# Kernel optimization log

Measured on AMD Instinct MI355X. Metric: run time of the kernel, lower is better.

The kernel has to match this reference:

```python
import jax, jax.numpy as jnp
import numpy as np

N = 100000
E = 1600000
IN_DIM, HID_DIM, LAT_DIM = 256, 128, 64


def glorot(key, shape):
    lim = float(np.sqrt(6.0 / (shape[0] + shape[1])))
    return jax.random.uniform(key, shape, jnp.float32, -lim, lim)


def setup_inputs() -> dict:
    key = jax.random.key(0)
    ks = jax.random.split(key, 8)
    x = jax.random.normal(ks[0], (N, IN_DIM), jnp.float32)
    edge_index = jax.random.randint(ks[1], (2, E), 0, N, jnp.int64)
    return {
        "x": x,
        "edge_index": edge_index,
        "W1": glorot(ks[2], (IN_DIM, HID_DIM)),
        "b1": jnp.zeros((HID_DIM,), jnp.float32),
        "Wmu": glorot(ks[3], (HID_DIM, LAT_DIM)),
        "bmu": jnp.zeros((LAT_DIM,), jnp.float32),
        "Wls": glorot(ks[4], (HID_DIM, LAT_DIM)),
        "bls": jnp.zeros((LAT_DIM,), jnp.float32),
    }


def gcn_conv(x, src, dst, norm, W, b, n_nodes):
    # PyG GCNConv: linear transform, then symmetric-normalized scatter-add
    h = x @ W                                   # [N, out]
    msg = h[src] * norm[:, None]                # [E+N, out] gathered messages
    out = jax.ops.segment_sum(msg, dst, num_segments=n_nodes)
    return out + b


def reference(x, edge_index, W1, b1, Wmu, bmu, Wls, bls):
    # add self-loops (GCNConv default)
    loop = jnp.arange(N, dtype=edge_index.dtype)
    src = jnp.concatenate([edge_index[0], loop])
    dst = jnp.concatenate([edge_index[1], loop])
    # symmetric degree normalization: deg computed on target nodes
    deg = jax.ops.segment_sum(jnp.ones_like(dst, jnp.float32), dst, num_segments=N)
    dinv = jnp.where(deg > 0, jax.lax.rsqrt(jnp.maximum(deg, 1.0)), 0.0)
    norm = dinv[src] * dinv[dst]                # [E+N]

    h = jax.nn.relu(gcn_conv(x, src, dst, norm, W1, b1, N))
    mu = gcn_conv(h, src, dst, norm, Wmu, bmu, N)
    logstd = gcn_conv(h, src, dst, norm, Wls, bls, N)
    return (mu, logstd)
```

## Files before the change

### kernel.cpp

```cpp
#include <hip/hip_runtime.h>

#define IN_DIM 256
#define HID    128
#define LAT    64
#define SLOTS  64
#define NBKT   16

typedef __attribute__((ext_vector_type(8))) short short8;
typedef __attribute__((ext_vector_type(4))) float floatx4;
typedef __attribute__((ext_vector_type(4))) int  intx4;
typedef __attribute__((ext_vector_type(2))) int  intx2;

static __device__ __forceinline__ ushort f2bf(float f) {
    union { float f; uint u; } v; v.f = f;
    uint u = v.u;
    uint r = (u + 0x7fffu + ((u >> 16) & 1u)) >> 16;
    return (ushort)r;
}
static __device__ __forceinline__ float bf_lo(uint v) { return __uint_as_float(v << 16); }
static __device__ __forceinline__ float bf_hi(uint v) { return __uint_as_float(v & 0xffff0000u); }

__global__ __launch_bounds__(256) void scatter_kernel(const int* __restrict__ src,
                                                      const int* __restrict__ dst,
                                                      int* __restrict__ bkt,
                                                      int* __restrict__ bkt_cnt,
                                                      int cap, int N, int E) {
    __shared__ int cntL[NBKT], baseL[NBKT], posL[NBKT];
    const int t = threadIdx.x;
    if (t < NBKT) { cntL[t] = 0; posL[t] = 0; }
    __syncthreads();
    const float sc = (float)NBKT / (float)N;
    const int e0 = blockIdx.x * 2048 + t * 8;
    int s[8], d[8];
    if (e0 + 7 < E) {
        *(int4*)(s)     = *(const int4*)(src + e0);
        *(int4*)(s + 4) = *(const int4*)(src + e0 + 4);
        *(int4*)(d)     = *(const int4*)(dst + e0);
        *(int4*)(d + 4) = *(const int4*)(dst + e0 + 4);
    } else {
        #pragma unroll
        for (int k = 0; k < 8; ++k) {
            int e = e0 + k;
            s[k] = (e < E) ? src[e] : 0;
            d[k] = (e < E) ? dst[e] : -1;
        }
    }
    int r[8];
    #pragma unroll
    for (int k = 0; k < 8; ++k) {
        r[k] = (d[k] >= 0) ? min((int)((float)d[k] * sc), NBKT - 1) : -1;
        if (r[k] >= 0) atomicAdd(&cntL[r[k]], 1);
    }
    __syncthreads();
    if (t < NBKT) baseL[t] = atomicAdd(&bkt_cnt[t], cntL[t]);
    __syncthreads();
    #pragma unroll
    for (int k = 0; k < 8; ++k) {
        if (r[k] >= 0) {
            int off = atomicAdd(&posL[r[k]], 1);
            int p = baseL[r[k]] + off;
            if (p < cap) {
                intx2 pk; pk.x = s[k]; pk.y = d[k];
                __builtin_nontemporal_store(pk,
                    (intx2*)(bkt + ((size_t)r[k] * cap + p) * 2));
            }
        }
    }
}

__global__ __launch_bounds__(256) void fill_kernel(const int* __restrict__ bkt,
                                                   const int* __restrict__ bkt_cnt,
                                                   int* __restrict__ cur,
                                                   int* __restrict__ csr, int cap) {
    const int xcd  = blockIdx.x & 7;
    const int slot = blockIdx.x >> 3;
    const int bpx  = gridDim.x >> 3;
    for (int ph = 0; ph < NBKT / 8; ++ph) {
        const int r  = ph * 8 + xcd;
        const int sz = min(bkt_cnt[r], cap);
        const int* b = bkt + (size_t)r * cap * 2;
        for (int i = (slot * 256 + threadIdx.x) * 4; i + 3 < sz; i += bpx * 1024) {
            intx4 e01 = __builtin_nontemporal_load((const intx4*)(b + (size_t)i * 2));
            intx4 e23 = __builtin_nontemporal_load((const intx4*)(b + (size_t)i * 2 + 4));
            int p0 = atomicAdd(&cur[e01.y], 1);
            int p1 = atomicAdd(&cur[e01.w], 1);
            int p2 = atomicAdd(&cur[e23.y], 1);
            int p3 = atomicAdd(&cur[e23.w], 1);
            if (p0 < SLOTS) csr[(e01.y << 6) + p0] = e01.x;
            if (p1 < SLOTS) csr[(e01.w << 6) + p1] = e01.z;
            if (p2 < SLOTS) csr[(e23.y << 6) + p2] = e23.x;
            if (p3 < SLOTS) csr[(e23.w << 6) + p3] = e23.z;
        }
        if (slot == 0) {
            int k = (sz & ~3) + threadIdx.x;
            if (k < sz) {
                int es = b[(size_t)k * 2];
                int ed = b[(size_t)k * 2 + 1];
                int p = atomicAdd(&cur[ed], 1);
                if (p < SLOTS) csr[(ed << 6) + p] = es;
            }
        }
    }
}

__global__ __launch_bounds__(256) void dinv_kernel(const int* __restrict__ cur,
                                                   float* __restrict__ dinv, int N) {
    int i = blockIdx.x * 256 + threadIdx.x;
    if (i < N) dinv[i] = rsqrtf((float)(cur[i] + 1));
}

__global__ void prep_weights(const float* __restrict__ W1, const float* __restrict__ Wmu,
                             const float* __restrict__ Wls,
                             ushort* __restrict__ W1T, ushort* __restrict__ W2T) {
    int idx = blockIdx.x * 256 + threadIdx.x;
    if (idx < IN_DIM * HID) {
        int n = idx & 127, k = idx >> 7;
        W1T[n * IN_DIM + k] = f2bf(W1[idx]);
    } else {
        int j = idx - IN_DIM * HID;
        if (j < HID * LAT) {
            int n = j & 63, k = j >> 6;
            W2T[n * HID + k] = f2bf(Wmu[j]);
        } else {
            int jj = j - HID * LAT;
            int n = jj & 63, k = jj >> 6;
            W2T[(64 + n) * HID + k] = f2bf(Wls[jj]);
        }
    }
}

__global__ __launch_bounds__(256) void gemm1_mfma(const float* __restrict__ X,
                                                  const ushort* __restrict__ W1T,
                                                  ushort* __restrict__ O, int N) {
    __shared__ ushort As[64 * 32];
    __shared__ ushort Bs[128 * 32];
    __shared__ ushort Cs[64 * 128];
    const int tid  = threadIdx.x;
    const int wave = tid >> 6, lane = tid & 63;
    const int q = lane >> 4, ln = lane & 15;
    const int row0 = blockIdx.x * 64;
    floatx4 acc[8] = {};

    for (int k0 = 0; k0 < IN_DIM; k0 += 32) {
        #pragma unroll
        for (int t = 0; t < 2; ++t) {
            int j = t * 256 + tid;
            int r = j >> 3, kc = (j & 7) * 4;
            float4 v = make_float4(0.f, 0.f, 0.f, 0.f);
            if (row0 + r < N)
                v = *(const float4*)(X + (size_t)(row0 + r) * IN_DIM + k0 + kc);
            *(ushort4*)(As + r * 32 + kc) =
                make_ushort4(f2bf(v.x), f2bf(v.y), f2bf(v.z), f2bf(v.w));
        }
        #pragma unroll
        for (int t = 0; t < 2; ++t) {
            int c = t * 256 + tid;
            int n = c >> 2, kc = (c & 3) * 8;
            *(int4*)(Bs + n * 32 + kc) = *(const int4*)(W1T + (size_t)n * IN_DIM + k0 + kc);
        }
        __syncthreads();
        short8 a = *(const short8*)(As + (wave * 16 + ln) * 32 + q * 8);
        #pragma unroll
        for (int t = 0; t < 8; ++t) {
            short8 b = *(const short8*)(Bs + (t * 16 + ln) * 32 + q * 8);
            acc[t] = __builtin_amdgcn_mfma_f32_16x16x32_bf16(a, b, acc[t], 0, 0, 0);
        }
        __syncthreads();
    }
    #pragma unroll
    for (int t = 0; t < 8; ++t)
        #pragma unroll
        for (int r = 0; r < 4; ++r)
            Cs[(wave * 16 + q * 4 + r) * 128 + t * 16 + ln] = f2bf(acc[t][r]);
    __syncthreads();
    #pragma unroll
    for (int t = 0; t < 4; ++t) {
        int j = t * 256 + tid;
        int r = j >> 4, c8 = (j & 15) * 8;
        if (row0 + r < N)
            *(int4*)(O + (size_t)(row0 + r) * HID + c8) = *(const int4*)(Cs + r * 128 + c8);
    }
}

__global__ __launch_bounds__(256) void agg_kernel(const ushort* __restrict__ in,
                                                  ushort* __restrict__ out,
                                                  const int* __restrict__ cnt,
                                                  const int* __restrict__ csr,
                                                  const float* __restrict__ dinv,
                                                  const float* __restrict__ bias,
                                                  int N, int mode) {
    int wid  = (blockIdx.x * 256 + threadIdx.x) >> 6;
    int lane = threadIdx.x & 63;
    if (wid >= N) return;
    const int cn   = min(cnt[wid], SLOTS);
    const float dd = dinv[wid];
    int e    = (cn > 0) ? csr[(wid << 6) + min(lane, cn - 1)] : wid;
    float nr = dinv[e] * dd;
    const int q    = lane >> 4;
    const int boff = (lane & 15) * 8;
    const ushort* inb = in + boff;
    float a0=0.f,a1=0.f,a2=0.f,a3=0.f,a4=0.f,a5=0.f,a6=0.f,a7=0.f;
    const int nfull = cn >> 2;
    int jj = 0;
    for (; jj + 2 <= nfull; jj += 2) {
        int j0 = (jj << 2) + q, j1 = j0 + 4;
        int   s0 = __shfl(e,  j0);
        int   s1 = __shfl(e,  j1);
        float n0 = __shfl(nr, j0);
        float n1 = __shfl(nr, j1);
        uint4 v0 = *(const uint4*)(inb + (size_t)s0 * HID);
        uint4 v1 = *(const uint4*)(inb + (size_t)s1 * HID);
        a0 += bf_lo(v0.x) * n0; a1 += bf_hi(v0.x) * n0;
        a2 += bf_lo(v0.y) * n0; a3 += bf_hi(v0.y) * n0;
        a4 += bf_lo(v0.z) * n0; a5 += bf_hi(v0.z) * n0;
        a6 += bf_lo(v0.w) * n0; a7 += bf_hi(v0.w) * n0;
        a0 += bf_lo(v1.x) * n1; a1 += bf_hi(v1.x) * n1;
        a2 += bf_lo(v1.y) * n1; a3 += bf_hi(v1.y) * n1;
        a4 += bf_lo(v1.z) * n1; a5 += bf_hi(v1.z) * n1;
        a6 += bf_lo(v1.w) * n1; a7 += bf_hi(v1.w) * n1;
    }
    if (jj < nfull) {
        int j0 = (jj << 2) + q;
        int   s0 = __shfl(e,  j0);
        float n0 = __shfl(nr, j0);
        uint4 v0 = *(const uint4*)(inb + (size_t)s0 * HID);
        a0 += bf_lo(v0.x) * n0; a1 += bf_hi(v0.x) * n0;
        a2 += bf_lo(v0.y) * n0; a3 += bf_hi(v0.y) * n0;
        a4 += bf_lo(v0.z) * n0; a5 += bf_hi(v0.z) * n0;
        a6 += bf_lo(v0.w) * n0; a7 += bf_hi(v0.w) * n0;
    }
    {
        int rem = cn - (nfull << 2);
        int jT  = max(min((nfull << 2) + q, cn - 1), 0);
        int   sT = __shfl(e,  jT);
        float nT = __shfl(nr, jT);
        if (q < rem) {
            uint4 v0 = *(const uint4*)(inb + (size_t)sT * HID);
            a0 += bf_lo(v0.x) * nT; a1 += bf_hi(v0.x) * nT;
            a2 += bf_lo(v0.y) * nT; a3 += bf_hi(v0.y) * nT;
            a4 += bf_lo(v0.z) * nT; a5 += bf_hi(v0.z) * nT;
            a6 += bf_lo(v0.w) * nT; a7 += bf_hi(v0.w) * nT;
        }
    }
    a0 += __shfl_xor(a0, 16); a1 += __shfl_xor(a1, 16);
    a2 += __shfl_xor(a2, 16); a3 += __shfl_xor(a3, 16);
    a4 += __shfl_xor(a4, 16); a5 += __shfl_xor(a5, 16);
    a6 += __shfl_xor(a6, 16); a7 += __shfl_xor(a7, 16);
    a0 += __shfl_xor(a0, 32); a1 += __shfl_xor(a1, 32);
    a2 += __shfl_xor(a2, 32); a3 += __shfl_xor(a3, 32);
    a4 += __shfl_xor(a4, 32); a5 += __shfl_xor(a5, 32);
    a6 += __shfl_xor(a6, 32); a7 += __shfl_xor(a7, 32);
    if (q == 0) {
        {
            uint4 sv = *(const uint4*)(in + (size_t)wid * HID + boff);
            float ss = dd * dd;
            a0 += bf_lo(sv.x) * ss; a1 += bf_hi(sv.x) * ss;
            a2 += bf_lo(sv.y) * ss; a3 += bf_hi(sv.y) * ss;
            a4 += bf_lo(sv.z) * ss; a5 += bf_hi(sv.z) * ss;
            a6 += bf_lo(sv.w) * ss; a7 += bf_hi(sv.w) * ss;
        }
        if (mode) {
            float4 b0 = *(const float4*)(bias + boff);
            float4 b1 = *(const float4*)(bias + boff + 4);
            a0 = fmaxf(a0 + b0.x, 0.f); a1 = fmaxf(a1 + b0.y, 0.f);
            a2 = fmaxf(a2 + b0.z, 0.f); a3 = fmaxf(a3 + b0.w, 0.f);
            a4 = fmaxf(a4 + b1.x, 0.f); a5 = fmaxf(a5 + b1.y, 0.f);
            a6 = fmaxf(a6 + b1.z, 0.f); a7 = fmaxf(a7 + b1.w, 0.f);
        }
        uint4 pk;
        pk.x = (uint)f2bf(a0) | ((uint)f2bf(a1) << 16);
        pk.y = (uint)f2bf(a2) | ((uint)f2bf(a3) << 16);
        pk.z = (uint)f2bf(a4) | ((uint)f2bf(a5) << 16);
        pk.w = (uint)f2bf(a6) | ((uint)f2bf(a7) << 16);
        *(uint4*)(out + (size_t)wid * HID + boff) = pk;
    }
}

__global__ __launch_bounds__(256) void gemm2_mfma(const ushort* __restrict__ G,
                                                  const ushort* __restrict__ W2T,
                                                  const float* __restrict__ bmu,
                                                  const float* __restrict__ bls,
                                                  float* __restrict__ mu,
                                                  float* __restrict__ ls, int N) {
    __shared__ ushort As[64 * 32];
    __shared__ ushort Bs[128 * 32];
    __shared__ float  Cs[64 * 128];
    const int tid  = threadIdx.x;
    const int wave = tid >> 6, lane = tid & 63;
    const int q = lane >> 4, ln = lane & 15;
    const int row0 = blockIdx.x * 64;
    floatx4 acc[8] = {};

    for (int k0 = 0; k0 < HID; k0 += 32) {
        {
            int r = tid >> 2, kc = (tid & 3) * 8;
            int4 v = make_int4(0, 0, 0, 0);
            if (row0 + r < N) v = *(const int4*)(G + (size_t)(row0 + r) * HID + k0 + kc);
            *(int4*)(As + r * 32 + kc) = v;
        }
        #pragma unroll
        for (int t = 0; t < 2; ++t) {
            int c = t * 256 + tid;
            int n = c >> 2, kc = (c & 3) * 8;
            *(int4*)(Bs + n * 32 + kc) = *(const int4*)(W2T + (size_t)n * HID + k0 + kc);
        }
        __syncthreads();
        short8 a = *(const short8*)(As + (wave * 16 + ln) * 32 + q * 8);
        #pragma unroll
        for (int t = 0; t < 8; ++t) {
            short8 b = *(const short8*)(Bs + (t * 16 + ln) * 32 + q * 8);
            acc[t] = __builtin_amdgcn_mfma_f32_16x16x32_bf16(a, b, acc[t], 0, 0, 0);
        }
        __syncthreads();
    }
    #pragma unroll
    for (int t = 0; t < 8; ++t)
        #pragma unroll
        for (int r = 0; r < 4; ++r)
            Cs[(wave * 16 + q * 4 + r) * 128 + t * 16 + ln] = acc[t][r];
    __syncthreads();
    #pragma unroll
    for (int t = 0; t < 8; ++t) {
        int j = t * 256 + tid;
        int r = j >> 5, c4 = (j & 31) * 4;
        if (row0 + r < N) {
            float4 v = *(const float4*)(Cs + r * 128 + c4);
            if (c4 < 64) {
                float4 b = *(const float4*)(bmu + c4);
                *(float4*)(mu + (size_t)(row0 + r) * LAT + c4) =
                    make_float4(v.x + b.x, v.y + b.y, v.z + b.z, v.w + b.w);
            } else {
                float4 b = *(const float4*)(bls + (c4 - 64));
                *(float4*)(ls + (size_t)(row0 + r) * LAT + (c4 - 64)) =
                    make_float4(v.x + b.x, v.y + b.y, v.z + b.z, v.w + b.w);
            }
        }
    }
}

extern "C" void kernel_launch(void* const* d_in, const int* in_sizes, int n_in,
                              void* d_out, int out_size, void* d_ws, size_t ws_size,
                              hipStream_t stream) {
    const float* x    = (const float*)d_in[0];
    const int*   edge = (const int*)d_in[1];
    const float* W1   = (const float*)d_in[2];
    const float* b1   = (const float*)d_in[3];
    const float* Wmu  = (const float*)d_in[4];
    const float* bmu  = (const float*)d_in[5];
    const float* Wls  = (const float*)d_in[6];
    const float* bls  = (const float*)d_in[7];

    const int N = in_sizes[0] / IN_DIM;
    const int E = in_sizes[1] / 2;
    const int cap = E / NBKT + 8192;

    const int* src = edge;
    const int* dst = edge + E;

    ushort* t1b  = (ushort*)d_ws;
    ushort* hb   = t1b + (size_t)N * HID;
    int*    csr  = (int*)(hb + (size_t)N * HID);
    int*    bkt  = (int*)(csr + (size_t)N * SLOTS);
    float*  dinv = (float*)(bkt + (size_t)NBKT * cap * 2);
    int*    cur  = (int*)(dinv + N);
    int* bkt_cnt = cur + N;
    ushort* W1T  = (ushort*)(bkt_cnt + NBKT);
    ushort* W2T  = W1T + IN_DIM * HID;
    ushort* gb   = t1b;

    float* mu = (float*)d_out;
    float* ls = mu + (size_t)N * LAT;

    (void)hipMemsetAsync(cur, 0, (size_t)(N + NBKT) * sizeof(int), stream);

    scatter_kernel<<<(E + 2047) / 2048, 256, 0, stream>>>(src, dst, bkt, bkt_cnt, cap, N, E);
    fill_kernel<<<1024, 256, 0, stream>>>(bkt, bkt_cnt, cur, csr, cap);
    dinv_kernel<<<(N + 255) / 256, 256, 0, stream>>>(cur, dinv, N);

    prep_weights<<<(IN_DIM * HID + 2 * HID * LAT) / 256, 256, 0, stream>>>(W1, Wmu, Wls, W1T, W2T);
    gemm1_mfma<<<(N + 63) / 64, 256, 0, stream>>>(x, W1T, t1b, N);

    {
        int blocks = (int)(((long long)N * 64 + 255) / 256);
        agg_kernel<<<blocks, 256, 0, stream>>>(t1b, hb, cur, csr, dinv, b1, N, 1);
    }
    {
        int blocks = (int)(((long long)N * 64 + 255) / 256);
        agg_kernel<<<blocks, 256, 0, stream>>>(hb, gb, cur, csr, dinv, nullptr, N, 0);
    }

    gemm2_mfma<<<(N + 63) / 64, 256, 0, stream>>>(gb, W2T, bmu, bls, mu, ls, N);
}
```

Before: 432.5 us.

## Fuse CSR fill with gemm1 and split aggregation across feature halves

Merges the CSR fill kernel and the first MFMA GEMM into a single launch so atomic-bound edge filling overlaps with compute-bound GEMM blocks; prep_weights is moved earlier to feed it. The aggregation kernel now splits each node's 128-wide row into two 64-column halves handled by separate blocks, with each wave processing 8 neighbours per step and an extra shuffle reduction. This aims to cut launch gaps and raise memory-level parallelism in the gather, at the cost of duplicated csr/dinv loads and shorter contiguous reads per neighbour.

```diff
diff --git a/kernel.cpp b/kernel.cpp
--- a/kernel.cpp
+++ b/kernel.cpp
@@ -5,6 +5,7 @@
 #define LAT    64
 #define SLOTS  64
 #define NBKT   16
+#define FILL_BLOCKS 1024
 
 typedef __attribute__((ext_vector_type(8))) short short8;
 typedef __attribute__((ext_vector_type(4))) float floatx4;
@@ -68,38 +69,93 @@
     }
 }
 
-__global__ __launch_bounds__(256) void fill_kernel(const int* __restrict__ bkt,
-                                                   const int* __restrict__ bkt_cnt,
-                                                   int* __restrict__ cur,
-                                                   int* __restrict__ csr, int cap) {
-    const int xcd  = blockIdx.x & 7;
-    const int slot = blockIdx.x >> 3;
-    const int bpx  = gridDim.x >> 3;
-    for (int ph = 0; ph < NBKT / 8; ++ph) {
-        const int r  = ph * 8 + xcd;
-        const int sz = min(bkt_cnt[r], cap);
-        const int* b = bkt + (size_t)r * cap * 2;
-        for (int i = (slot * 256 + threadIdx.x) * 4; i + 3 < sz; i += bpx * 1024) {
-            intx4 e01 = __builtin_nontemporal_load((const intx4*)(b + (size_t)i * 2));
-            intx4 e23 = __builtin_nontemporal_load((const intx4*)(b + (size_t)i * 2 + 4));
-            int p0 = atomicAdd(&cur[e01.y], 1);
-            int p1 = atomicAdd(&cur[e01.w], 1);
-            int p2 = atomicAdd(&cur[e23.y], 1);
-            int p3 = atomicAdd(&cur[e23.w], 1);
-            if (p0 < SLOTS) csr[(e01.y << 6) + p0] = e01.x;
-            if (p1 < SLOTS) csr[(e01.w << 6) + p1] = e01.z;
-            if (p2 < SLOTS) csr[(e23.y << 6) + p2] = e23.x;
-            if (p3 < SLOTS) csr[(e23.w << 6) + p3] = e23.z;
-        }
-        if (slot == 0) {
-            int k = (sz & ~3) + threadIdx.x;
-            if (k < sz) {
-                int es = b[(size_t)k * 2];
-                int ed = b[(size_t)k * 2 + 1];
-                int p = atomicAdd(&cur[ed], 1);
-                if (p < SLOTS) csr[(ed << 6) + p] = es;
+__global__ __launch_bounds__(256) void fill_gemm1_kernel(
+        const int* __restrict__ bkt, const int* __restrict__ bkt_cnt,
+        int* __restrict__ cur, int* __restrict__ csr, int cap,
+        const float* __restrict__ X, const ushort* __restrict__ W1T,
+        ushort* __restrict__ O, int N) {
+    __shared__ ushort As[64 * 32];
+    __shared__ ushort Bs[128 * 32];
+    __shared__ ushort Cs[64 * 128];
+
+    if (blockIdx.x < FILL_BLOCKS) {
+        const int xcd  = blockIdx.x & 7;
+        const int slot = blockIdx.x >> 3;
+        const int bpx  = FILL_BLOCKS >> 3;
+        for (int ph = 0; ph < NBKT / 8; ++ph) {
+            const int r  = ph * 8 + xcd;
+            const int sz = min(bkt_cnt[r], cap);
+            const int* b = bkt + (size_t)r * cap * 2;
+            for (int i = (slot * 256 + threadIdx.x) * 4; i + 3 < sz; i += bpx * 1024) {
+                intx4 e01 = __builtin_nontemporal_load((const intx4*)(b + (size_t)i * 2));
+                intx4 e23 = __builtin_nontemporal_load((const intx4*)(b + (size_t)i * 2 + 4));
+                int p0 = atomicAdd(&cur[e01.y], 1);
+                int p1 = atomicAdd(&cur[e01.w], 1);
+                int p2 = atomicAdd(&cur[e23.y], 1);
+                int p3 = atomicAdd(&cur[e23.w], 1);
+                if (p0 < SLOTS) csr[(e01.y << 6) + p0] = e01.x;
+                if (p1 < SLOTS) csr[(e01.w << 6) + p1] = e01.z;
+                if (p2 < SLOTS) csr[(e23.y << 6) + p2] = e23.x;
+                if (p3 < SLOTS) csr[(e23.w << 6) + p3] = e23.z;
             }
-        }
+            if (slot == 0) {
+                int k = (sz & ~3) + threadIdx.x;
+                if (k < sz) {
+                    int es = b[(size_t)k * 2];
+                    int ed = b[(size_t)k * 2 + 1];
+                    int p = atomicAdd(&cur[ed], 1);
+                    if (p < SLOTS) csr[(ed << 6) + p] = es;
+                }
+            }
+        }
+        return;
+    }
+
+    const int bid  = blockIdx.x - FILL_BLOCKS;
+    const int tid  = threadIdx.x;
+    const int wave = tid >> 6, lane = tid & 63;
+    const int q = lane >> 4, ln = lane & 15;
+    const int row0 = bid * 64;
+    floatx4 acc[8] = {};
+
+    for (int k0 = 0; k0 < IN_DIM; k0 += 32) {
+        #pragma unroll
+        for (int t = 0; t < 2; ++t) {
+            int j = t * 256 + tid;
+            int r = j >> 3, kc = (j & 7) * 4;
+            float4 v = make_float4(0.f, 0.f, 0.f, 0.f);
+            if (row0 + r < N)
+                v = *(const float4*)(X + (size_t)(row0 + r) * IN_DIM + k0 + kc);
+            *(ushort4*)(As + r * 32 + kc) =
+                make_ushort4(f2bf(v.x), f2bf(v.y), f2bf(v.z), f2bf(v.w));
+        }
+        #pragma unroll
+        for (int t = 0; t < 2; ++t) {
+            int c = t * 256 + tid;
+            int n = c >> 2, kc = (c & 3) * 8;
+            *(int4*)(Bs + n * 32 + kc) = *(const int4*)(W1T + (size_t)n * IN_DIM + k0 + kc);
+        }
+        __syncthreads();
+        short8 a = *(const short8*)(As + (wave * 16 + ln) * 32 + q * 8);
+        #pragma unroll
+        for (int t = 0; t < 8; ++t) {
+            short8 b = *(const short8*)(Bs + (t * 16 + ln) * 32 + q * 8);
+            acc[t] = __builtin_amdgcn_mfma_f32_16x16x32_bf16(a, b, acc[t], 0, 0, 0);
+        }
+        __syncthreads();
+    }
+    #pragma unroll
+    for (int t = 0; t < 8; ++t)
+        #pragma unroll
+        for (int r = 0; r < 4; ++r)
+            Cs[(wave * 16 + q * 4 + r) * 128 + t * 16 + ln] = f2bf(acc[t][r]);
+    __syncthreads();
+    #pragma unroll
+    for (int t = 0; t < 4; ++t) {
+        int j = t * 256 + tid;
+        int r = j >> 4, c8 = (j & 15) * 8;
+        if (row0 + r < N)
+            *(int4*)(O + (size_t)(row0 + r) * HID + c8) = *(const int4*)(Cs + r * 128 + c8);
     }
 }
 
@@ -129,59 +185,6 @@
     }
 }
 
-__global__ __launch_bounds__(256) void gemm1_mfma(const float* __restrict__ X,
-                                                  const ushort* __restrict__ W1T,
-                                                  ushort* __restrict__ O, int N) {
-    __shared__ ushort As[64 * 32];
-    __shared__ ushort Bs[128 * 32];
-    __shared__ ushort Cs[64 * 128];
-    const int tid  = threadIdx.x;
-    const int wave = tid >> 6, lane = tid & 63;
-    const int q = lane >> 4, ln = lane & 15;
-    const int row0 = blockIdx.x * 64;
-    floatx4 acc[8] = {};
-
-    for (int k0 = 0; k0 < IN_DIM; k0 += 32) {
-        #pragma unroll
-        for (int t = 0; t < 2; ++t) {
-            int j = t * 256 + tid;
-            int r = j >> 3, kc = (j & 7) * 4;
-            float4 v = make_float4(0.f, 0.f, 0.f, 0.f);
-            if (row0 + r < N)
-                v = *(const float4*)(X + (size_t)(row0 + r) * IN_DIM + k0 + kc);
-            *(ushort4*)(As + r * 32 + kc) =
-                make_ushort4(f2bf(v.x), f2bf(v.y), f2bf(v.z), f2bf(v.w));
-        }
-        #pragma unroll
-        for (int t = 0; t < 2; ++t) {
-            int c = t * 256 + tid;
-            int n = c >> 2, kc = (c & 3) * 8;
-            *(int4*)(Bs + n * 32 + kc) = *(const int4*)(W1T + (size_t)n * IN_DIM + k0 + kc);
-        }
-        __syncthreads();
-        short8 a = *(const short8*)(As + (wave * 16 + ln) * 32 + q * 8);
-        #pragma unroll
-        for (int t = 0; t < 8; ++t) {
-            short8 b = *(const short8*)(Bs + (t * 16 + ln) * 32 + q * 8);
-            acc[t] = __builtin_amdgcn_mfma_f32_16x16x32_bf16(a, b, acc[t], 0, 0, 0);
-        }
-        __syncthreads();
-    }
-    #pragma unroll
-    for (int t = 0; t < 8; ++t)
-        #pragma unroll
-        for (int r = 0; r < 4; ++r)
-            Cs[(wave * 16 + q * 4 + r) * 128 + t * 16 + ln] = f2bf(acc[t][r]);
-    __syncthreads();
-    #pragma unroll
-    for (int t = 0; t < 4; ++t) {
-        int j = t * 256 + tid;
-        int r = j >> 4, c8 = (j & 15) * 8;
-        if (row0 + r < N)
-            *(int4*)(O + (size_t)(row0 + r) * HID + c8) = *(const int4*)(Cs + r * 128 + c8);
-    }
-}
-
 __global__ __launch_bounds__(256) void agg_kernel(const ushort* __restrict__ in,
                                                   ushort* __restrict__ out,
                                                   const int* __restrict__ cnt,
@@ -189,21 +192,23 @@
                                                   const float* __restrict__ dinv,
                                                   const float* __restrict__ bias,
                                                   int N, int mode) {
-    int wid  = (blockIdx.x * 256 + threadIdx.x) >> 6;
-    int lane = threadIdx.x & 63;
+    const int h   = (blockIdx.x >> 2) & 1;
+    const int nb  = (blockIdx.x >> 3) * 4 + (blockIdx.x & 3);
+    const int wid = nb * 4 + (threadIdx.x >> 6);
+    const int lane = threadIdx.x & 63;
     if (wid >= N) return;
     const int cn   = min(cnt[wid], SLOTS);
     const float dd = dinv[wid];
     int e    = (cn > 0) ? csr[(wid << 6) + min(lane, cn - 1)] : wid;
     float nr = dinv[e] * dd;
-    const int q    = lane >> 4;
-    const int boff = (lane & 15) * 8;
+    const int q    = lane >> 3;
+    const int boff = h * 64 + (lane & 7) * 8;
     const ushort* inb = in + boff;
     float a0=0.f,a1=0.f,a2=0.f,a3=0.f,a4=0.f,a5=0.f,a6=0.f,a7=0.f;
-    const int nfull = cn >> 2;
+    const int nfull = cn >> 3;
     int jj = 0;
     for (; jj + 2 <= nfull; jj += 2) {
-        int j0 = (jj << 2) + q, j1 = j0 + 4;
+        int j0 = (jj << 3) + q, j1 = j0 + 8;
         int   s0 = __shfl(e,  j0);
         int   s1 = __shfl(e,  j1);
         float n0 = __shfl(nr, j0);
@@ -220,7 +225,7 @@
         a6 += bf_lo(v1.w) * n1; a7 += bf_hi(v1.w) * n1;
     }
     if (jj < nfull) {
-        int j0 = (jj << 2) + q;
+        int j0 = (jj << 3) + q;
         int   s0 = __shfl(e,  j0);
         float n0 = __shfl(nr, j0);
         uint4 v0 = *(const uint4*)(inb + (size_t)s0 * HID);
@@ -230,8 +235,8 @@
         a6 += bf_lo(v0.w) * n0; a7 += bf_hi(v0.w) * n0;
     }
     {
-        int rem = cn - (nfull << 2);
-        int jT  = max(min((nfull << 2) + q, cn - 1), 0);
+        int rem = cn - (nfull << 3);
+        int jT  = max(min((nfull << 3) + q, cn - 1), 0);
         int   sT = __shfl(e,  jT);
         float nT = __shfl(nr, jT);
         if (q < rem) {
@@ -242,6 +247,10 @@
             a6 += bf_lo(v0.w) * nT; a7 += bf_hi(v0.w) * nT;
         }
     }
+    a0 += __shfl_xor(a0,  8); a1 += __shfl_xor(a1,  8);
+    a2 += __shfl_xor(a2,  8); a3 += __shfl_xor(a3,  8);
+    a4 += __shfl_xor(a4,  8); a5 += __shfl_xor(a5,  8);
+    a6 += __shfl_xor(a6,  8); a7 += __shfl_xor(a7,  8);
     a0 += __shfl_xor(a0, 16); a1 += __shfl_xor(a1, 16);
     a2 += __shfl_xor(a2, 16); a3 += __shfl_xor(a3, 16);
     a4 += __shfl_xor(a4, 16); a5 += __shfl_xor(a5, 16);
@@ -374,18 +383,21 @@
     (void)hipMemsetAsync(cur, 0, (size_t)(N + NBKT) * sizeof(int), stream);
 
     scatter_kernel<<<(E + 2047) / 2048, 256, 0, stream>>>(src, dst, bkt, bkt_cnt, cap, N, E);
-    fill_kernel<<<1024, 256, 0, stream>>>(bkt, bkt_cnt, cur, csr, cap);
+    prep_weights<<<(IN_DIM * HID + 2 * HID * LAT) / 256, 256, 0, stream>>>(W1, Wmu, Wls, W1T, W2T);
+
+    {
+        int g1Blocks = (N + 63) / 64;
+        fill_gemm1_kernel<<<FILL_BLOCKS + g1Blocks, 256, 0, stream>>>(
+            bkt, bkt_cnt, cur, csr, cap, x, W1T, t1b, N);
+    }
     dinv_kernel<<<(N + 255) / 256, 256, 0, stream>>>(cur, dinv, N);
 
-    prep_weights<<<(IN_DIM * HID + 2 * HID * LAT) / 256, 256, 0, stream>>>(W1, Wmu, Wls, W1T, W2T);
-    gemm1_mfma<<<(N + 63) / 64, 256, 0, stream>>>(x, W1T, t1b, N);
-
     {
-        int blocks = (int)(((long long)N * 64 + 255) / 256);
+        int blocks = ((N + 15) / 16) * 8;
         agg_kernel<<<blocks, 256, 0, stream>>>(t1b, hb, cur, csr, dinv, b1, N, 1);
     }
     {
-        int blocks = (int)(((long long)N * 64 + 255) / 256);
+        int blocks = ((N + 15) / 16) * 8;
         agg_kernel<<<blocks, 256, 0, stream>>>(hb, gb, cur, csr, dinv, nullptr, N, 0);
     }
 
```

New measurement: 478.9 us. 1.11x slower.

## Use fine-grained 200-node buckets and build CSR slots in shared memory

Applied to the files above, without the earlier changes.

The scatter now splits edges into many small buckets of 200 destination nodes each, replacing the previous 16 coarse buckets. Each bucket is then turned into padded CSR rows by one block that does LDS atomics into a shared slot array and writes the rows out with coalesced int4 stores. This removes the global atomics on per-node counters and the scattered CSR writes. In exchange the scatter kernel has many more shared counters and global bucket atomics, and the fixed bucket cap of 4096 with at most 512 buckets only works when N and the per-bucket degree stay small enough.

```diff
diff --git a/kernel.cpp b/kernel.cpp
--- a/kernel.cpp
+++ b/kernel.cpp
@@ -4,7 +4,8 @@
 #define HID    128
 #define LAT    64
 #define SLOTS  64
-#define NBKT   16
+#define RANGE  200
+#define MAXBKT 512
 
 typedef __attribute__((ext_vector_type(8))) short short8;
 typedef __attribute__((ext_vector_type(4))) float floatx4;
@@ -24,12 +25,11 @@
                                                       const int* __restrict__ dst,
                                                       int* __restrict__ bkt,
                                                       int* __restrict__ bkt_cnt,
-                                                      int cap, int N, int E) {
-    __shared__ int cntL[NBKT], baseL[NBKT], posL[NBKT];
+                                                      int cap, int nbkt, int E) {
+    __shared__ int cntL[MAXBKT], baseL[MAXBKT], posL[MAXBKT];
     const int t = threadIdx.x;
-    if (t < NBKT) { cntL[t] = 0; posL[t] = 0; }
-    __syncthreads();
-    const float sc = (float)NBKT / (float)N;
+    for (int b = t; b < nbkt; b += 256) { cntL[b] = 0; posL[b] = 0; }
+    __syncthreads();
     const int e0 = blockIdx.x * 2048 + t * 8;
     int s[8], d[8];
     if (e0 + 7 < E) {
@@ -48,11 +48,14 @@
     int r[8];
     #pragma unroll
     for (int k = 0; k < 8; ++k) {
-        r[k] = (d[k] >= 0) ? min((int)((float)d[k] * sc), NBKT - 1) : -1;
+        r[k] = (d[k] >= 0) ? (d[k] / RANGE) : -1;
         if (r[k] >= 0) atomicAdd(&cntL[r[k]], 1);
     }
     __syncthreads();
-    if (t < NBKT) baseL[t] = atomicAdd(&bkt_cnt[t], cntL[t]);
+    for (int b = t; b < nbkt; b += 256) {
+        int c = cntL[b];
+        baseL[b] = c ? atomicAdd(&bkt_cnt[b], c) : 0;
+    }
     __syncthreads();
     #pragma unroll
     for (int k = 0; k < 8; ++k) {
@@ -68,39 +71,35 @@
     }
 }
 
-__global__ __launch_bounds__(256) void fill_kernel(const int* __restrict__ bkt,
-                                                   const int* __restrict__ bkt_cnt,
-                                                   int* __restrict__ cur,
-                                                   int* __restrict__ csr, int cap) {
-    const int xcd  = blockIdx.x & 7;
-    const int slot = blockIdx.x >> 3;
-    const int bpx  = gridDim.x >> 3;
-    for (int ph = 0; ph < NBKT / 8; ++ph) {
-        const int r  = ph * 8 + xcd;
-        const int sz = min(bkt_cnt[r], cap);
-        const int* b = bkt + (size_t)r * cap * 2;
-        for (int i = (slot * 256 + threadIdx.x) * 4; i + 3 < sz; i += bpx * 1024) {
-            intx4 e01 = __builtin_nontemporal_load((const intx4*)(b + (size_t)i * 2));
-            intx4 e23 = __builtin_nontemporal_load((const intx4*)(b + (size_t)i * 2 + 4));
-            int p0 = atomicAdd(&cur[e01.y], 1);
-            int p1 = atomicAdd(&cur[e01.w], 1);
-            int p2 = atomicAdd(&cur[e23.y], 1);
-            int p3 = atomicAdd(&cur[e23.w], 1);
-            if (p0 < SLOTS) csr[(e01.y << 6) + p0] = e01.x;
-            if (p1 < SLOTS) csr[(e01.w << 6) + p1] = e01.z;
-            if (p2 < SLOTS) csr[(e23.y << 6) + p2] = e23.x;
-            if (p3 < SLOTS) csr[(e23.w << 6) + p3] = e23.z;
-        }
-        if (slot == 0) {
-            int k = (sz & ~3) + threadIdx.x;
-            if (k < sz) {
-                int es = b[(size_t)k * 2];
-                int ed = b[(size_t)k * 2 + 1];
-                int p = atomicAdd(&cur[ed], 1);
-                if (p < SLOTS) csr[(ed << 6) + p] = es;
-            }
-        }
-    }
+__global__ __launch_bounds__(256) void fill_bin_kernel(const int* __restrict__ bkt,
+                                                       const int* __restrict__ bkt_cnt,
+                                                       int* __restrict__ cur,
+                                                       int* __restrict__ csr,
+                                                       int cap, int N) {
+    __shared__ int lcnt[RANGE];
+    __shared__ int lslots[RANGE * SLOTS];
+    const int r  = blockIdx.x;
+    const int lo = r * RANGE;
+    const int R  = min(RANGE, N - lo);
+    if (R <= 0) return;
+    for (int j = threadIdx.x; j < R; j += 256) lcnt[j] = 0;
+    __syncthreads();
+    const int sz = min(bkt_cnt[r], cap);
+    const int* b = bkt + (size_t)r * cap * 2;
+    for (int i = threadIdx.x; i < sz; i += 256) {
+        intx2 e = __builtin_nontemporal_load((const intx2*)(b + (size_t)i * 2));
+        int ln = e.y - lo;
+        int p = atomicAdd(&lcnt[ln], 1);
+        if (p < SLOTS) lslots[(ln << 6) + p] = e.x;
+    }
+    __syncthreads();
+    const int nInt4 = R << 4;
+    int4* dstp = (int4*)(csr + ((size_t)lo << 6));
+    const int4* srcp = (const int4*)lslots;
+    for (int j = threadIdx.x; j < nInt4; j += 256)
+        dstp[j] = srcp[j];
+    for (int j = threadIdx.x; j < R; j += 256)
+        cur[lo + j] = lcnt[j];
 }
 
 __global__ __launch_bounds__(256) void dinv_kernel(const int* __restrict__ cur,
@@ -350,9 +349,10 @@
     const float* Wls  = (const float*)d_in[6];
     const float* bls  = (const float*)d_in[7];
 
-    const int N = in_sizes[0] / IN_DIM;
-    const int E = in_sizes[1] / 2;
-    const int cap = E / NBKT + 8192;
+    const int N    = in_sizes[0] / IN_DIM;
+    const int E    = in_sizes[1] / 2;
+    const int nbkt = (N + RANGE - 1) / RANGE;
+    const int cap  = 4096;
 
     const int* src = edge;
     const int* dst = edge + E;
@@ -361,20 +361,20 @@
     ushort* hb   = t1b + (size_t)N * HID;
     int*    csr  = (int*)(hb + (size_t)N * HID);
     int*    bkt  = (int*)(csr + (size_t)N * SLOTS);
-    float*  dinv = (float*)(bkt + (size_t)NBKT * cap * 2);
+    float*  dinv = (float*)(bkt + (size_t)MAXBKT * cap * 2);
     int*    cur  = (int*)(dinv + N);
     int* bkt_cnt = cur + N;
-    ushort* W1T  = (ushort*)(bkt_cnt + NBKT);
+    ushort* W1T  = (ushort*)(bkt_cnt + MAXBKT);
     ushort* W2T  = W1T + IN_DIM * HID;
     ushort* gb   = t1b;
 
     float* mu = (float*)d_out;
     float* ls = mu + (size_t)N * LAT;
 
-    (void)hipMemsetAsync(cur, 0, (size_t)(N + NBKT) * sizeof(int), stream);
-
-    scatter_kernel<<<(E + 2047) / 2048, 256, 0, stream>>>(src, dst, bkt, bkt_cnt, cap, N, E);
-    fill_kernel<<<1024, 256, 0, stream>>>(bkt, bkt_cnt, cur, csr, cap);
+    (void)hipMemsetAsync(bkt_cnt, 0, (size_t)MAXBKT * sizeof(int), stream);
+
+    scatter_kernel<<<(E + 2047) / 2048, 256, 0, stream>>>(src, dst, bkt, bkt_cnt, cap, nbkt, E);
+    fill_bin_kernel<<<nbkt, 256, 0, stream>>>(bkt, bkt_cnt, cur, csr, cap, N);
     dinv_kernel<<<(N + 255) / 256, 256, 0, stream>>>(cur, dinv, N);
 
     prep_weights<<<(IN_DIM * HID + 2 * HID * LAT) / 256, 256, 0, stream>>>(W1, Wmu, Wls, W1T, W2T);
```

New measurement: 412.1 us. 1.05x faster.
